# Optimization experiments

Hardware: AMD Instinct MI355X
Metric: run time of the kernel (lower is better)

The kernel has to match this reference:

```python
import jax, jax.numpy as jnp
import numpy as np

B, H, T, D, R = 2, 12, 2048, 64, 16
D_STD = D - R


def setup_inputs() -> dict:
    key = jax.random.key(0)
    ks = jax.random.split(key, 5)
    return {
        "Q": jax.random.normal(ks[0], (B, H, T, D), jnp.float32),
        "K": jax.random.normal(ks[1], (B, H, T, D), jnp.float32),
        "V": jax.random.normal(ks[2], (B, H, T, D), jnp.float32),
        "d_bias": jax.random.normal(ks[3], (B, H, T), jnp.float32),
        "W_recip": jax.random.normal(ks[4], (D, R), jnp.float32) * 0.02,
        "w_std": jnp.full((H,), 0.5, jnp.float32),
        "w_rec": jnp.full((H,), 0.3, jnp.float32),
        "w_disc": jnp.full((H,), 0.2, jnp.float32),
    }


def reference(Q, K, V, d_bias, W_recip, w_std, w_rec, w_disc):
    b, h, t, d = Q.shape
    r = W_recip.shape[1]
    d_std = d - r
    sq_std = jnp.sqrt(w_std)[None, :, None, None]  # [1,H,1,1]
    sq_rec = jnp.sqrt(w_rec)[None, :, None, None]
    Q_low = jnp.einsum("bhtd,dr->bhtr", Q, W_recip)  # [B,H,T,R]
    K_low = jnp.einsum("bhtd,dr->bhtr", K, W_recip)
    Q_aug = jnp.concatenate([sq_std * Q[..., :d_std], sq_rec * K_low], axis=-1)  # [B,H,T,D]
    K_aug = jnp.concatenate([sq_std * K[..., :d_std], sq_rec * Q_low], axis=-1)
    scale = 1.0 / jnp.sqrt(jnp.asarray(d, Q.dtype))
    scores = jnp.einsum("bhqd,bhkd->bhqk", Q_aug, K_aug) * scale  # [B,H,T,T]
    # rank-1 additive bias, broadcast over queries: bias[b,h,q,k] = w_disc[h]*d_bias[b,h,k]
    scores = scores + (w_disc[None, :, None, None] * d_bias[:, :, None, :])
    causal = jnp.tril(jnp.ones((t, t), bool))  # [T,T]
    scores = jnp.where(causal[None, None], scores, -jnp.inf)
    attn = jax.nn.softmax(scores, axis=-1)
    return jnp.einsum("bhqk,bhkd->bhqd", attn, V)
```

## Files before the change

kernel.cpp:

```cpp
#include <hip/hip_runtime.h>
#include <math.h>

#define T_SEQ 2048
#define NH    12
#define NB    2
#define BHC   (NB*NH)
#define NQT   32

typedef _Float16 half4_t __attribute__((ext_vector_type(4)));
typedef _Float16 half8_t __attribute__((ext_vector_type(8)));
typedef float    floatx4 __attribute__((ext_vector_type(4)));

__device__ __forceinline__ void async_cp16(const void* g, void* l) {
  __builtin_amdgcn_global_load_lds((const __attribute__((address_space(1))) void*)g,
                                   (__attribute__((address_space(3))) void*)l, 16, 0, 0);
}
__device__ __forceinline__ void async_cp4(const void* g, void* l) {
  __builtin_amdgcn_global_load_lds((const __attribute__((address_space(1))) void*)g,
                                   (__attribute__((address_space(3))) void*)l, 4, 0, 0);
}

__global__ __launch_bounds__(256) void prep_kernel(
    const float* __restrict__ Q, const float* __restrict__ K,
    const float* __restrict__ V, const float* __restrict__ W,
    const float* __restrict__ wstd, const float* __restrict__ wrec,
    ushort* __restrict__ QF, ushort* __restrict__ KF, ushort* __restrict__ VF)
{
  __shared__ __align__(16) float Qs[64*72];
  __shared__ __align__(16) float Ks[64*72];
  __shared__ __align__(16) float Vs[64*72];
  __shared__ __align__(16) float Lq[64*20];
  __shared__ __align__(16) float Lk[64*20];

  const int tid = threadIdx.x;
  const int w = tid >> 6, lane = tid & 63;
  const int quad = lane >> 4, ln = lane & 15;
  const int bh = blockIdx.x >> 5;
  const int tblk = blockIdx.x & 31;
  const long g0 = ((long)bh * T_SEQ + tblk * 64) * 64;

  const float4* gQ = (const float4*)(Q + g0);
  const float4* gK = (const float4*)(K + g0);
  const float4* gV = (const float4*)(V + g0);
  for (int i = tid; i < 1024; i += 256) {
    int r = i >> 4, c = i & 15;
    *(float4*)&Qs[r*72 + c*4] = gQ[i];
    *(float4*)&Ks[r*72 + c*4] = gK[i];
    *(float4*)&Vs[r*72 + c*4] = gV[i];
  }
  __syncthreads();

  half4_t bw[4];
#pragma unroll
  for (int dk = 0; dk < 4; dk++)
#pragma unroll
    for (int i = 0; i < 4; i++)
      bw[dk][i] = (_Float16)W[(dk*16 + quad*4 + i)*16 + ln];

  floatx4 cq = {0.f,0.f,0.f,0.f}, ck = {0.f,0.f,0.f,0.f};
#pragma unroll
  for (int dk = 0; dk < 4; dk++) {
    half4_t aq, ak;
#pragma unroll
    for (int i = 0; i < 4; i++) {
      aq[i] = (_Float16)Qs[(w*16 + ln)*72 + dk*16 + quad*4 + i];
      ak[i] = (_Float16)Ks[(w*16 + ln)*72 + dk*16 + quad*4 + i];
    }
    cq = __builtin_amdgcn_mfma_f32_16x16x16f16(aq, bw[dk], cq, 0, 0, 0);
    ck = __builtin_amdgcn_mfma_f32_16x16x16f16(ak, bw[dk], ck, 0, 0, 0);
  }
#pragma unroll
  for (int i = 0; i < 4; i++) {
    Lq[(w*16 + quad*4 + i)*20 + ln] = cq[i];
    Lk[(w*16 + quad*4 + i)*20 + ln] = ck[i];
  }
  __syncthreads();

  const int h = bh % NH;
  const float sstd = sqrtf(wstd[h]);
  const float srec = sqrtf(wrec[h]);
  const float qsc  = 0.125f;

#pragma unroll
  for (int cc = 0; cc < 2; cc++) {
    int c = tid + cc*256;
    {
      int lp = c & 63, dp = (c >> 6) & 1, rt = c >> 7;
      int lnp = lp & 15, qp = lp >> 4;
      int row = rt*16 + lnp;
      half8_t hq, hk;
#pragma unroll
      for (int uu = 0; uu < 2; uu++) {
        int d0 = dp*32 + uu*16 + qp*4;
        if (d0 < 48) {
#pragma unroll
          for (int j = 0; j < 4; j++) {
            hq[uu*4+j] = (_Float16)(qsc*sstd*Qs[row*72 + d0 + j]);
            hk[uu*4+j] = (_Float16)(sstd*Ks[row*72 + d0 + j]);
          }
        } else {
#pragma unroll
          for (int j = 0; j < 4; j++) {
            hq[uu*4+j] = (_Float16)(qsc*srec*Lk[row*20 + d0-48 + j]);
            hk[uu*4+j] = (_Float16)(srec*Lq[row*20 + d0-48 + j]);
          }
        }
      }
      long tile16 = (long)bh*128 + tblk*4 + rt;
      ((int4*)QF)[tile16*128 + dp*64 + lp] = *(int4*)&hq;
      ((int4*)KF)[tile16*128 + dp*64 + lp] = *(int4*)&hk;
    }
    {
      int lv = c & 63, nt = (c >> 6) & 3, v2 = c >> 8;
      int lnv = lv & 15, qv = lv >> 4;
      int d = nt*16 + lnv;
      half8_t hv;
#pragma unroll
      for (int j = 0; j < 4; j++) {
        hv[j]   = (_Float16)Vs[(v2*32 + qv*4 + j)*72 + d];
        hv[4+j] = (_Float16)Vs[(v2*32 + 16 + qv*4 + j)*72 + d];
      }
      long t64 = (long)bh*32 + tblk;
      ((int4*)VF)[t64*512 + (v2*4 + nt)*64 + lv] = *(int4*)&hv;
    }
  }
}

__global__ __launch_bounds__(256) void flash_kernel(
    const ushort* __restrict__ QF, const ushort* __restrict__ KF,
    const ushort* __restrict__ VF, const float* __restrict__ dbias,
    const float* __restrict__ wdisc, float* __restrict__ Out)
{
  __shared__ __align__(16) ushort KsL[4096];
  __shared__ __align__(16) ushort VsL[4096];
  __shared__ float bs[64];

  const int tid = threadIdx.x;
  const int w = tid >> 6, lane = tid & 63;
  const int quad = lane >> 4, ln = lane & 15;
  const int bid = blockIdx.x;
  const int bh = bid % BHC;
  const int qt = NQT - 1 - bid / BHC;
  const int h = bh % NH;
  const int q0 = qt * 64;
  const int qrow = q0 + w*16 + ln;
  const float wd = wdisc[h];

  half4_t bq[4];
  {
    const ushort* gQ = QF + ((long)bh*128 + qt*4 + w) * 1024;
    half8_t q01 = *(const half8_t*)(gQ + lane*8);
    half8_t q23 = *(const half8_t*)(gQ + 512 + lane*8);
    bq[0] = __builtin_shufflevector(q01, q01, 0,1,2,3);
    bq[1] = __builtin_shufflevector(q01, q01, 4,5,6,7);
    bq[2] = __builtin_shufflevector(q23, q23, 0,1,2,3);
    bq[3] = __builtin_shufflevector(q23, q23, 4,5,6,7);
  }

  float m_i = -1e30f, l_i = 0.f;
  floatx4 acc[4];
#pragma unroll
  for (int nt = 0; nt < 4; nt++) acc[nt] = (floatx4){0.f,0.f,0.f,0.f};

  for (int kt = 0; kt <= qt; kt++) {
    __syncthreads();
    {
      const ushort* gK = KF + ((long)bh*256 + (long)kt*8) * 512;
      const ushort* gV = VF + ((long)bh*256 + (long)kt*8) * 512;
      for (int c = w; c < 8; c += 4) {
        async_cp16(gK + c*512 + lane*8, &KsL[c*512]);
        async_cp16(gV + c*512 + lane*8, &VsL[c*512]);
      }
      if (w == 0) async_cp4(dbias + (long)bh*T_SEQ + kt*64 + lane, bs);
    }
    __syncthreads();

    floatx4 st[4];
#pragma unroll
    for (int mt = 0; mt < 4; mt++) st[mt] = (floatx4){0.f,0.f,0.f,0.f};
#pragma unroll
    for (int mt = 0; mt < 4; mt++) {
#pragma unroll
      for (int dp = 0; dp < 2; dp++) {
        half8_t kk = *(const half8_t*)&KsL[(mt*2 + dp)*512 + lane*8];
        half4_t a0 = __builtin_shufflevector(kk, kk, 0,1,2,3);
        half4_t a1 = __builtin_shufflevector(kk, kk, 4,5,6,7);
        st[mt] = __builtin_amdgcn_mfma_f32_16x16x16f16(a0, bq[2*dp],   st[mt], 0, 0, 0);
        st[mt] = __builtin_amdgcn_mfma_f32_16x16x16f16(a1, bq[2*dp+1], st[mt], 0, 0, 0);
      }
    }

    const bool diag = (kt == qt);
    float rowmax = -1e30f;
#pragma unroll
    for (int mt = 0; mt < 4; mt++)
#pragma unroll
      for (int i = 0; i < 4; i++) {
        float v = st[mt][i] + wd * bs[mt*16 + quad*4 + i];
        int key = kt*64 + mt*16 + quad*4 + i;
        if (diag && key > qrow) v = -1e30f;
        st[mt][i] = v;
        rowmax = fmaxf(rowmax, v);
      }
    rowmax = fmaxf(rowmax, __shfl_xor(rowmax, 16));
    rowmax = fmaxf(rowmax, __shfl_xor(rowmax, 32));
    float mnew  = fmaxf(m_i, rowmax);
    float alpha = __expf(m_i - mnew);
    float psum = 0.f;
    half4_t pa[4];
#pragma unroll
    for (int mt = 0; mt < 4; mt++)
#pragma unroll
      for (int i = 0; i < 4; i++) {
        float p = __expf(st[mt][i] - mnew);
        psum += p;
        pa[mt][i] = (_Float16)p;
      }
    psum += __shfl_xor(psum, 16);
    psum += __shfl_xor(psum, 32);
    l_i = l_i * alpha + psum;
    m_i = mnew;

    float af[4];
#pragma unroll
    for (int i = 0; i < 4; i++) af[i] = __shfl(alpha, quad*4 + i);
#pragma unroll
    for (int nt = 0; nt < 4; nt++)
#pragma unroll
      for (int i = 0; i < 4; i++) acc[nt][i] *= af[i];

#pragma unroll
    for (int v2 = 0; v2 < 2; v2++)
#pragma unroll
      for (int nt = 0; nt < 4; nt++) {
        half8_t vv = *(const half8_t*)&VsL[(v2*4 + nt)*512 + lane*8];
        half4_t b0 = __builtin_shufflevector(vv, vv, 0,1,2,3);
        half4_t b1 = __builtin_shufflevector(vv, vv, 4,5,6,7);
        acc[nt] = __builtin_amdgcn_mfma_f32_16x16x16f16(pa[2*v2],   b0, acc[nt], 0, 0, 0);
        acc[nt] = __builtin_amdgcn_mfma_f32_16x16x16f16(pa[2*v2+1], b1, acc[nt], 0, 0, 0);
      }
  }

  float lr[4];
#pragma unroll
  for (int i = 0; i < 4; i++) lr[i] = 1.f / __shfl(l_i, quad*4 + i);
  const long obase = (long)bh*T_SEQ*64 + (long)(q0 + w*16)*64;
#pragma unroll
  for (int i = 0; i < 4; i++)
#pragma unroll
    for (int nt = 0; nt < 4; nt++)
      Out[obase + (quad*4 + i)*64 + nt*16 + ln] = acc[nt][i] * lr[i];
}

extern "C" void kernel_launch(void* const* d_in, const int* in_sizes, int n_in,
                              void* d_out, int out_size, void* d_ws, size_t ws_size,
                              hipStream_t stream) {
  const float* Q     = (const float*)d_in[0];
  const float* K     = (const float*)d_in[1];
  const float* V     = (const float*)d_in[2];
  const float* dbias = (const float*)d_in[3];
  const float* W     = (const float*)d_in[4];
  const float* wstd  = (const float*)d_in[5];
  const float* wrec  = (const float*)d_in[6];
  const float* wdisc = (const float*)d_in[7];
  float* Out = (float*)d_out;

  const long NEL = (long)BHC * T_SEQ * 64;
  ushort* QF = (ushort*)d_ws;
  ushort* KF = QF + NEL;
  ushort* VF = KF + NEL;

  prep_kernel<<<BHC * NQT, 256, 0, stream>>>(Q, K, V, W, wstd, wrec, QF, KF, VF);
  flash_kernel<<<BHC * NQT, 256, 0, stream>>>(QF, KF, VF, dbias, wdisc, Out);
}
```

Baseline: 145.8 us.

## Double-buffer K/V tiles in flash loop, use 16x16x32 MFMA, fp16 prep staging

The flash kernel now double-buffers the K, V and bias tiles in LDS. The next tile's async global-to-LDS copy is issued before computing on the current one, which removes one barrier per iteration and overlaps load latency with compute. QK^T now uses the 16x16x32 f16 MFMA with 8-element operands, and the prep kernel packs Q/K with a matching contiguous-k layout. The prep kernel stages inputs in LDS as fp16 and scales with vector multiplies. The costs are doubled LDS use in the flash kernel, scaling done in fp16 rather than fp32, and reliance on the barrier to wait for outstanding async copies.

```diff
diff --git a/kernel.cpp b/kernel.cpp
--- a/kernel.cpp
+++ b/kernel.cpp
@@ -18,6 +18,9 @@
 __device__ __forceinline__ void async_cp4(const void* g, void* l) {
   __builtin_amdgcn_global_load_lds((const __attribute__((address_space(1))) void*)g,
                                    (__attribute__((address_space(3))) void*)l, 4, 0, 0);
+}
+__device__ __forceinline__ half8_t h8splat(_Float16 s) {
+  return (half8_t){s, s, s, s, s, s, s, s};
 }
 
 __global__ __launch_bounds__(256) void prep_kernel(
@@ -26,27 +29,27 @@
     const float* __restrict__ wstd, const float* __restrict__ wrec,
     ushort* __restrict__ QF, ushort* __restrict__ KF, ushort* __restrict__ VF)
 {
-  __shared__ __align__(16) float Qs[64*72];
-  __shared__ __align__(16) float Ks[64*72];
-  __shared__ __align__(16) float Vs[64*72];
-  __shared__ __align__(16) float Lq[64*20];
-  __shared__ __align__(16) float Lk[64*20];
+  __shared__ __align__(16) _Float16 Qsh[64*72];
+  __shared__ __align__(16) _Float16 Ksh[64*72];
+  __shared__ __align__(16) _Float16 Vsh[64*72];
+  __shared__ __align__(16) _Float16 Lqh[64*16];
+  __shared__ __align__(16) _Float16 Lkh[64*16];
 
   const int tid = threadIdx.x;
   const int w = tid >> 6, lane = tid & 63;
   const int quad = lane >> 4, ln = lane & 15;
-  const int bh = blockIdx.x >> 5;
-  const int tblk = blockIdx.x & 31;
+  const int bh = blockIdx.x >> 5, tblk = blockIdx.x & 31;
   const long g0 = ((long)bh * T_SEQ + tblk * 64) * 64;
 
   const float4* gQ = (const float4*)(Q + g0);
   const float4* gK = (const float4*)(K + g0);
   const float4* gV = (const float4*)(V + g0);
   for (int i = tid; i < 1024; i += 256) {
-    int r = i >> 4, c = i & 15;
-    *(float4*)&Qs[r*72 + c*4] = gQ[i];
-    *(float4*)&Ks[r*72 + c*4] = gK[i];
-    *(float4*)&Vs[r*72 + c*4] = gV[i];
+    int r = i >> 4, c4 = i & 15;
+    float4 q = gQ[i], k = gK[i], v = gV[i];
+    *(half4_t*)&Qsh[r*72 + c4*4] = (half4_t){(_Float16)q.x,(_Float16)q.y,(_Float16)q.z,(_Float16)q.w};
+    *(half4_t*)&Ksh[r*72 + c4*4] = (half4_t){(_Float16)k.x,(_Float16)k.y,(_Float16)k.z,(_Float16)k.w};
+    *(half4_t*)&Vsh[r*72 + c4*4] = (half4_t){(_Float16)v.x,(_Float16)v.y,(_Float16)v.z,(_Float16)v.w};
   }
   __syncthreads();
 
@@ -60,51 +63,40 @@
   floatx4 cq = {0.f,0.f,0.f,0.f}, ck = {0.f,0.f,0.f,0.f};
 #pragma unroll
   for (int dk = 0; dk < 4; dk++) {
-    half4_t aq, ak;
-#pragma unroll
-    for (int i = 0; i < 4; i++) {
-      aq[i] = (_Float16)Qs[(w*16 + ln)*72 + dk*16 + quad*4 + i];
-      ak[i] = (_Float16)Ks[(w*16 + ln)*72 + dk*16 + quad*4 + i];
-    }
+    half4_t aq = *(const half4_t*)&Qsh[(w*16 + ln)*72 + dk*16 + quad*4];
+    half4_t ak = *(const half4_t*)&Ksh[(w*16 + ln)*72 + dk*16 + quad*4];
     cq = __builtin_amdgcn_mfma_f32_16x16x16f16(aq, bw[dk], cq, 0, 0, 0);
     ck = __builtin_amdgcn_mfma_f32_16x16x16f16(ak, bw[dk], ck, 0, 0, 0);
   }
 #pragma unroll
   for (int i = 0; i < 4; i++) {
-    Lq[(w*16 + quad*4 + i)*20 + ln] = cq[i];
-    Lk[(w*16 + quad*4 + i)*20 + ln] = ck[i];
+    Lqh[(w*16 + quad*4 + i)*16 + ln] = (_Float16)cq[i];
+    Lkh[(w*16 + quad*4 + i)*16 + ln] = (_Float16)ck[i];
   }
   __syncthreads();
 
   const int h = bh % NH;
   const float sstd = sqrtf(wstd[h]);
   const float srec = sqrtf(wrec[h]);
-  const float qsc  = 0.125f;
+  const half8_t hq_std = h8splat((_Float16)(0.125f * sstd));
+  const half8_t hk_std = h8splat((_Float16)sstd);
+  const half8_t hq_rec = h8splat((_Float16)(0.125f * srec));
+  const half8_t hk_rec = h8splat((_Float16)srec);
 
 #pragma unroll
   for (int cc = 0; cc < 2; cc++) {
-    int c = tid + cc*256;
+    int c = tid + cc * 256;
     {
       int lp = c & 63, dp = (c >> 6) & 1, rt = c >> 7;
-      int lnp = lp & 15, qp = lp >> 4;
-      int row = rt*16 + lnp;
+      int row = rt*16 + (lp & 15);
+      int d0 = dp*32 + (lp >> 4)*8;
       half8_t hq, hk;
-#pragma unroll
-      for (int uu = 0; uu < 2; uu++) {
-        int d0 = dp*32 + uu*16 + qp*4;
-        if (d0 < 48) {
-#pragma unroll
-          for (int j = 0; j < 4; j++) {
-            hq[uu*4+j] = (_Float16)(qsc*sstd*Qs[row*72 + d0 + j]);
-            hk[uu*4+j] = (_Float16)(sstd*Ks[row*72 + d0 + j]);
-          }
-        } else {
-#pragma unroll
-          for (int j = 0; j < 4; j++) {
-            hq[uu*4+j] = (_Float16)(qsc*srec*Lk[row*20 + d0-48 + j]);
-            hk[uu*4+j] = (_Float16)(srec*Lq[row*20 + d0-48 + j]);
-          }
-        }
+      if (d0 < 48) {
+        hq = *(const half8_t*)&Qsh[row*72 + d0] * hq_std;
+        hk = *(const half8_t*)&Ksh[row*72 + d0] * hk_std;
+      } else {
+        hq = *(const half8_t*)&Lkh[row*16 + (d0-48)] * hq_rec;
+        hk = *(const half8_t*)&Lqh[row*16 + (d0-48)] * hk_rec;
       }
       long tile16 = (long)bh*128 + tblk*4 + rt;
       ((int4*)QF)[tile16*128 + dp*64 + lp] = *(int4*)&hq;
@@ -112,16 +104,14 @@
     }
     {
       int lv = c & 63, nt = (c >> 6) & 3, v2 = c >> 8;
-      int lnv = lv & 15, qv = lv >> 4;
-      int d = nt*16 + lnv;
+      int d = nt*16 + (lv & 15), qv = lv >> 4;
       half8_t hv;
 #pragma unroll
       for (int j = 0; j < 4; j++) {
-        hv[j]   = (_Float16)Vs[(v2*32 + qv*4 + j)*72 + d];
-        hv[4+j] = (_Float16)Vs[(v2*32 + 16 + qv*4 + j)*72 + d];
-      }
-      long t64 = (long)bh*32 + tblk;
-      ((int4*)VF)[t64*512 + (v2*4 + nt)*64 + lv] = *(int4*)&hv;
+        hv[j]   = Vsh[(v2*32 + qv*4 + j)*72 + d];
+        hv[4+j] = Vsh[(v2*32 + 16 + qv*4 + j)*72 + d];
+      }
+      ((int4*)VF)[((long)bh*32 + tblk)*512 + (v2*4 + nt)*64 + lv] = *(int4*)&hv;
     }
   }
 }
@@ -131,9 +121,9 @@
     const ushort* __restrict__ VF, const float* __restrict__ dbias,
     const float* __restrict__ wdisc, float* __restrict__ Out)
 {
-  __shared__ __align__(16) ushort KsL[4096];
-  __shared__ __align__(16) ushort VsL[4096];
-  __shared__ float bs[64];
+  __shared__ __align__(16) ushort KsL[2][4096];
+  __shared__ __align__(16) ushort VsL[2][4096];
+  __shared__ float bs[2][64];
 
   const int tid = threadIdx.x;
   const int w = tid >> 6, lane = tid & 63;
@@ -146,15 +136,15 @@
   const int qrow = q0 + w*16 + ln;
   const float wd = wdisc[h];
 
-  half4_t bq[4];
+  const ushort* gKb = KF + ((long)bh*256) * 512;
+  const ushort* gVb = VF + ((long)bh*256) * 512;
+  const float*  gB  = dbias + (long)bh*T_SEQ;
+
+  half8_t bq[2];
   {
     const ushort* gQ = QF + ((long)bh*128 + qt*4 + w) * 1024;
-    half8_t q01 = *(const half8_t*)(gQ + lane*8);
-    half8_t q23 = *(const half8_t*)(gQ + 512 + lane*8);
-    bq[0] = __builtin_shufflevector(q01, q01, 0,1,2,3);
-    bq[1] = __builtin_shufflevector(q01, q01, 4,5,6,7);
-    bq[2] = __builtin_shufflevector(q23, q23, 0,1,2,3);
-    bq[3] = __builtin_shufflevector(q23, q23, 4,5,6,7);
+    bq[0] = *(const half8_t*)(gQ + lane*8);
+    bq[1] = *(const half8_t*)(gQ + 512 + lane*8);
   }
 
   float m_i = -1e30f, l_i = 0.f;
@@ -162,33 +152,37 @@
 #pragma unroll
   for (int nt = 0; nt < 4; nt++) acc[nt] = (floatx4){0.f,0.f,0.f,0.f};
 
+  {
+    for (int c = w; c < 8; c += 4) {
+      async_cp16(gKb + c*512 + lane*8, &KsL[0][c*512]);
+      async_cp16(gVb + c*512 + lane*8, &VsL[0][c*512]);
+    }
+    if (w == 0) async_cp4(gB + lane, &bs[0][0]);
+  }
+
   for (int kt = 0; kt <= qt; kt++) {
+    const int cur = kt & 1;
     __syncthreads();
-    {
-      const ushort* gK = KF + ((long)bh*256 + (long)kt*8) * 512;
-      const ushort* gV = VF + ((long)bh*256 + (long)kt*8) * 512;
+
+    if (kt < qt) {
+      const long o = (long)(kt + 1) * 8 * 512;
       for (int c = w; c < 8; c += 4) {
-        async_cp16(gK + c*512 + lane*8, &KsL[c*512]);
-        async_cp16(gV + c*512 + lane*8, &VsL[c*512]);
-      }
-      if (w == 0) async_cp4(dbias + (long)bh*T_SEQ + kt*64 + lane, bs);
-    }
-    __syncthreads();
+        async_cp16(gKb + o + c*512 + lane*8, &KsL[1-cur][c*512]);
+        async_cp16(gVb + o + c*512 + lane*8, &VsL[1-cur][c*512]);
+      }
+      if (w == 0) async_cp4(gB + (kt+1)*64 + lane, &bs[1-cur][0]);
+    }
 
     floatx4 st[4];
 #pragma unroll
     for (int mt = 0; mt < 4; mt++) st[mt] = (floatx4){0.f,0.f,0.f,0.f};
 #pragma unroll
-    for (int mt = 0; mt < 4; mt++) {
+    for (int mt = 0; mt < 4; mt++)
 #pragma unroll
       for (int dp = 0; dp < 2; dp++) {
-        half8_t kk = *(const half8_t*)&KsL[(mt*2 + dp)*512 + lane*8];
-        half4_t a0 = __builtin_shufflevector(kk, kk, 0,1,2,3);
-        half4_t a1 = __builtin_shufflevector(kk, kk, 4,5,6,7);
-        st[mt] = __builtin_amdgcn_mfma_f32_16x16x16f16(a0, bq[2*dp],   st[mt], 0, 0, 0);
-        st[mt] = __builtin_amdgcn_mfma_f32_16x16x16f16(a1, bq[2*dp+1], st[mt], 0, 0, 0);
-      }
-    }
+        half8_t a = *(const half8_t*)&KsL[cur][(mt*2 + dp)*512 + lane*8];
+        st[mt] = __builtin_amdgcn_mfma_f32_16x16x32_f16(a, bq[dp], st[mt], 0, 0, 0);
+      }
 
     const bool diag = (kt == qt);
     float rowmax = -1e30f;
@@ -196,7 +190,7 @@
     for (int mt = 0; mt < 4; mt++)
 #pragma unroll
       for (int i = 0; i < 4; i++) {
-        float v = st[mt][i] + wd * bs[mt*16 + quad*4 + i];
+        float v = st[mt][i] + wd * bs[cur][mt*16 + quad*4 + i];
         int key = kt*64 + mt*16 + quad*4 + i;
         if (diag && key > qrow) v = -1e30f;
         st[mt][i] = v;
@@ -233,7 +227,7 @@
     for (int v2 = 0; v2 < 2; v2++)
 #pragma unroll
       for (int nt = 0; nt < 4; nt++) {
-        half8_t vv = *(const half8_t*)&VsL[(v2*4 + nt)*512 + lane*8];
+        half8_t vv = *(const half8_t*)&VsL[cur][(v2*4 + nt)*512 + lane*8];
         half4_t b0 = __builtin_shufflevector(vv, vv, 0,1,2,3);
         half4_t b1 = __builtin_shufflevector(vv, vv, 4,5,6,7);
         acc[nt] = __builtin_amdgcn_mfma_f32_16x16x16f16(pa[2*v2],   b0, acc[nt], 0, 0, 0);
```

Result: faster. 142.0 us (-2.6%).
